# Kernel tuning notes

Measured on AMD Instinct MI355X. Metric: run time of the kernel, lower is better.

## Reference

```python
import jax, jax.numpy as jnp
import numpy as np

N_NODES = 100000
N_EDGES = 1200000
NDIM_IN = 64
EDIMS = 64
NDIM_OUT = 64


def setup_inputs() -> dict:
    key = jax.random.key(0)
    k = jax.random.split(key, 8)
    nfeats = jax.random.normal(k[0], (N_NODES, NDIM_IN), dtype=jnp.float32)
    efeats = jax.random.normal(k[1], (N_EDGES, EDIMS), dtype=jnp.float32)
    src = jax.random.randint(k[2], (N_EDGES,), 0, N_NODES)
    dst = jax.random.randint(k[3], (N_EDGES,), 0, N_NODES)
    # Linear layers: y = x @ W + b, W stored [in, out]
    s_msg = 1.0 / np.sqrt(NDIM_IN + EDIMS)
    s_app = 1.0 / np.sqrt(NDIM_IN + NDIM_OUT)
    W_msg = jax.random.normal(k[4], (NDIM_IN + EDIMS, NDIM_OUT), dtype=jnp.float32) * s_msg
    b_msg = jnp.zeros((NDIM_OUT,), dtype=jnp.float32)
    W_apply = jax.random.normal(k[5], (NDIM_IN + NDIM_OUT, NDIM_OUT), dtype=jnp.float32) * s_app
    b_apply = jnp.zeros((NDIM_OUT,), dtype=jnp.float32)
    return {"nfeats": nfeats, "efeats": efeats, "src": src, "dst": dst,
            "W_msg": W_msg, "b_msg": b_msg, "W_apply": W_apply, "b_apply": b_apply}


def reference(nfeats, efeats, src, dst, W_msg, b_msg, W_apply, b_apply):
    # per-edge message: W_msg(cat[h_src, e_h])  -> [E, ndim_out]
    msg_in = jnp.concatenate([nfeats[src], efeats], axis=1)  # [E, ndim_in+edims]
    m = msg_in @ W_msg + b_msg                                # [E, ndim_out]
    # mean aggregation over destination nodes (DGL fn.mean; 0 for isolated nodes)
    msum = jax.ops.segment_sum(m, dst, num_segments=N_NODES)  # [N, ndim_out]
    deg = jax.ops.segment_sum(jnp.ones((m.shape[0], 1), m.dtype), dst,
                              num_segments=N_NODES)           # [N, 1]
    h_neigh = jnp.where(deg > 0, msum / jnp.maximum(deg, 1.0), 0.0)
    # node update: relu(W_apply(cat[h, h_neigh]))
    h = jax.nn.relu(jnp.concatenate([nfeats, h_neigh], axis=1) @ W_apply + b_apply)
    return h
```

## Files before the change

kernel.cpp:

```cpp
#include <hip/hip_runtime.h>

#define N_NODES 100000
#define N_EDGES 1200000
#define D 64
#define SLOTS 48

typedef float    f32x4 __attribute__((ext_vector_type(4)));
typedef _Float16 f16x4 __attribute__((ext_vector_type(4)));


__global__ __launch_bounds__(256) void init_kernel(
    int4* __restrict__ zp, const float* __restrict__ nfeats,
    const float* __restrict__ W_msg, const float* __restrict__ b_msg,
    const float* __restrict__ W_apply, float* __restrict__ Wf,
    float* __restrict__ c1, _Float16* __restrict__ nf16)
{
    int b = blockIdx.x;
    if (b < 98) {
        int i = b * 256 + threadIdx.x;
        if (i < 25000) zp[i] = make_int4(0, 0, 0, 0);
    } else if (b < 227) {
        if (threadIdx.x < 64) {
            int i = b - 98;
            int j = threadIdx.x;
            float acc = 0.f;
            if (i < 128) {
                for (int k = 0; k < 64; ++k)
                    acc = fmaf(W_msg[i * 64 + k], W_apply[(64 + k) * 64 + j], acc);
                Wf[i * 64 + j] = acc;
            } else {
                for (int k = 0; k < 64; ++k)
                    acc = fmaf(b_msg[k], W_apply[(64 + k) * 64 + j], acc);
                c1[j] = acc;
            }
        }
    } else {
        size_t i = (size_t)(b - 227) * 256 + threadIdx.x;
        if (i < (size_t)N_NODES * 16) {
            f32x4 v = *(const f32x4*)(nfeats + i * 4);
            f16x4 h;
            h[0] = (_Float16)v[0]; h[1] = (_Float16)v[1];
            h[2] = (_Float16)v[2]; h[3] = (_Float16)v[3];
            *(f16x4*)(nf16 + i * 4) = h;
        }
    }
}

__global__ __launch_bounds__(256) void scatter_kernel(
    const int* __restrict__ src, const int* __restrict__ dst,
    int* __restrict__ cursor, int2* __restrict__ idx_s)
{
    int e = blockIdx.x * 256 + threadIdx.x;
    if (e >= N_EDGES) return;
    int d = __builtin_nontemporal_load(dst + e);
    int s = __builtin_nontemporal_load(src + e);
    int pos = atomicAdd(&cursor[d], 1);
    if (pos < SLOTS) idx_s[(size_t)d * SLOTS + pos] = make_int2(e, s);
}

__global__ __launch_bounds__(256) void gather_kernel(
    const _Float16* __restrict__ nf16, const float* __restrict__ efeats,
    const int2* __restrict__ idx_s, const int* __restrict__ cursor,
    float* __restrict__ agg_h, float* __restrict__ agg_e)
{
    int w = (int)((blockIdx.x * blockDim.x + threadIdx.x) >> 6);
    int lane = threadIdx.x & 63;
    if (w >= N_NODES) return;
    int r  = lane >> 4;
    int c4 = (lane & 15) << 2;
    const int2* bucket = idx_s + (size_t)w * SLOTS;
    int dgi = min(__builtin_amdgcn_readfirstlane(cursor[w]), SLOTS);
    f32x4 sh = (f32x4)0.f;
    f32x4 se = (f32x4)0.f;
    int full = dgi & ~7;
    for (int i = 0; i < full; i += 8) {
        int2 pA = bucket[i + r];
        int2 pB = bucket[i + 4 + r];
        f32x4 eA = __builtin_nontemporal_load((const f32x4*)(efeats + (size_t)pA.x * D + c4));
        f32x4 eB = __builtin_nontemporal_load((const f32x4*)(efeats + (size_t)pB.x * D + c4));
        f16x4 hA = *(const f16x4*)(nf16 + (size_t)pA.y * D + c4);
        f16x4 hB = *(const f16x4*)(nf16 + (size_t)pB.y * D + c4);
        se += eA + eB;
        #pragma unroll
        for (int q = 0; q < 4; ++q) sh[q] += (float)hA[q] + (float)hB[q];
    }
    if (full < dgi) {
        int iA = full + r, iB = full + 4 + r;
        float mA = (iA < dgi) ? 1.f : 0.f;
        float mB = (iB < dgi) ? 1.f : 0.f;
        int2 pA = bucket[(iA < dgi) ? iA : 0];
        int2 pB = bucket[(iB < dgi) ? iB : 0];
        f32x4 eA = __builtin_nontemporal_load((const f32x4*)(efeats + (size_t)pA.x * D + c4));
        f32x4 eB = __builtin_nontemporal_load((const f32x4*)(efeats + (size_t)pB.x * D + c4));
        f16x4 hA = *(const f16x4*)(nf16 + (size_t)pA.y * D + c4);
        f16x4 hB = *(const f16x4*)(nf16 + (size_t)pB.y * D + c4);
        #pragma unroll
        for (int q = 0; q < 4; ++q) {
            se[q] = fmaf(mA, eA[q], se[q]); sh[q] = fmaf(mA, (float)hA[q], sh[q]);
            se[q] = fmaf(mB, eB[q], se[q]); sh[q] = fmaf(mB, (float)hB[q], sh[q]);
        }
    }
    #pragma unroll
    for (int m = 16; m <= 32; m <<= 1) {
        #pragma unroll
        for (int q = 0; q < 4; ++q) {
            sh[q] += __shfl_xor(sh[q], m);
            se[q] += __shfl_xor(se[q], m);
        }
    }
    if (r == 0)       *(f32x4*)(agg_h + (size_t)w * D + c4) = sh;
    else if (r == 1)  *(f32x4*)(agg_e + (size_t)w * D + c4) = se;
}

__global__ __launch_bounds__(256) void node_update_kernel(
    const float* __restrict__ nfeats, const float* __restrict__ W_apply,
    const float* __restrict__ b_apply, const float* __restrict__ Wf,
    const float* __restrict__ c1, const float* __restrict__ agg_e,
    const int* __restrict__ deg, float* out )
{
    __shared__ float sX[64 * 17];
    __shared__ float sOut[64 * 65];
    int t = threadIdx.x;
    int l = t & 63;
    int jg = __builtin_amdgcn_readfirstlane(t >> 6);
    int node0 = blockIdx.x * 64;
    int node = min(node0 + l, N_NODES - 1);
    int dgi = deg[node];
    float s = dgi > 0 ? 1.f / (float)dgi : 0.f;
    float gate = dgi > 0 ? 1.f : 0.f;

    float accN[16], accX[16];
    #pragma unroll
    for (int j = 0; j < 16; ++j) { accN[j] = 0.f; accX[j] = 0.f; }

    #define STAGE(srcp, kp)                                                   \
    {                                                                         \
        int row = t >> 2, kq = t & 3;                                         \
        int grow = min(node0 + row, N_NODES - 1);                             \
        f32x4 v = *(const f32x4*)((srcp) + (size_t)grow * D + (kp) + kq * 4); \
        sX[row * 17 + kq * 4 + 0] = v[0];                                     \
        sX[row * 17 + kq * 4 + 1] = v[1];                                     \
        sX[row * 17 + kq * 4 + 2] = v[2];                                     \
        sX[row * 17 + kq * 4 + 3] = v[3];                                     \
    }

    #define ACCUM(acc, Wp, kw0)                                               \
    {                                                                         \
        _Pragma("unroll")                                                     \
        for (int g = 0; g < 4; ++g) {                                         \
            float x0 = sX[l * 17 + g * 4 + 0];                                \
            float x1 = sX[l * 17 + g * 4 + 1];                                \
            float x2 = sX[l * 17 + g * 4 + 2];                                \
            float x3 = sX[l * 17 + g * 4 + 3];                                \
            const float* w0 = (Wp) + (size_t)((kw0) + g * 4 + 0) * 64 + jg * 16; \
            const float* w1 = (Wp) + (size_t)((kw0) + g * 4 + 1) * 64 + jg * 16; \
            const float* w2 = (Wp) + (size_t)((kw0) + g * 4 + 2) * 64 + jg * 16; \
            const float* w3 = (Wp) + (size_t)((kw0) + g * 4 + 3) * 64 + jg * 16; \
            _Pragma("unroll")                                                 \
            for (int jj = 0; jj < 16; ++jj) {                                 \
                acc[jj] = fmaf(x0, w0[jj], acc[jj]);                          \
                acc[jj] = fmaf(x1, w1[jj], acc[jj]);                          \
                acc[jj] = fmaf(x2, w2[jj], acc[jj]);                          \
                acc[jj] = fmaf(x3, w3[jj], acc[jj]);                          \
            }                                                                 \
        }                                                                     \
    }

    for (int p = 0; p < 4; ++p) {
        STAGE(nfeats, p * 16);
        __syncthreads();
        ACCUM(accN, W_apply, p * 16);
        __syncthreads();
    }
    for (int p = 0; p < 8; ++p) {
        const float* srcp = (p < 4) ? out : agg_e;
        STAGE(srcp, (p & 3) * 16);
        __syncthreads();
        ACCUM(accX, Wf, p * 16);
        __syncthreads();
    }

    #pragma unroll
    for (int jj = 0; jj < 16; ++jj) {
        int j = jg * 16 + jj;
        sOut[l * 65 + j] = fmaxf(accN[jj] + s * accX[jj] + gate * c1[j] + b_apply[j], 0.f);
    }
    __syncthreads();

    #pragma unroll
    for (int rr = 0; rr < 16; ++rr) {
        int row = jg * 16 + rr;
        int nd = node0 + row;
        if (nd < N_NODES) out[(size_t)nd * D + l] = sOut[row * 65 + l];
    }
    #undef STAGE
    #undef ACCUM
}

extern "C" void kernel_launch(void* const* d_in, const int* in_sizes, int n_in,
                              void* d_out, int out_size, void* d_ws, size_t ws_size,
                              hipStream_t stream) {
    const float* nfeats  = (const float*)d_in[0];
    const float* efeats  = (const float*)d_in[1];
    const int*   src     = (const int*)d_in[2];
    const int*   dst     = (const int*)d_in[3];
    const float* W_msg   = (const float*)d_in[4];
    const float* b_msg   = (const float*)d_in[5];
    const float* W_apply = (const float*)d_in[6];
    const float* b_apply = (const float*)d_in[7];
    float* out = (float*)d_out;

    int*      cursor = (int*)d_ws;
    float*    Wf     = (float*)(cursor + 100352);
    float*    c1     = Wf + 128 * 64;
    _Float16* nf16   = (_Float16*)(c1 + 64);
    int2*     idx_s  = (int2*)(nf16 + (size_t)N_NODES * D);
    float*    agg_e  = (float*)(idx_s + (size_t)N_NODES * SLOTS);

    init_kernel<<<98 + 129 + 6250, 256, 0, stream>>>(
        (int4*)d_ws, nfeats, W_msg, b_msg, W_apply, Wf, c1, nf16);

    int eb = (N_EDGES + 255) / 256;
    scatter_kernel<<<eb, 256, 0, stream>>>(src, dst, cursor, idx_s);

    gather_kernel<<<N_NODES / 4, 256, 0, stream>>>(
        nf16, efeats, idx_s, cursor, out , agg_e);

    node_update_kernel<<<(N_NODES + 63) / 64, 256, 0, stream>>>(
        nfeats, W_apply, b_apply, Wf, c1, agg_e, cursor, out);
}
```

Before: 217.4 us.

## Fuse node update into gather and precompute the self-feature projection in init

The self term nfeats@W_apply+b_apply is now computed in the init kernel, alongside the fp16 conversion, and written to a Qa buffer. The separate node_update kernel is removed. Each gather wave now multiplies its aggregated sums by the fused Wf matrix held in LDS, using cross-lane shuffles, and writes the final relu output directly. This drops a kernel launch and the round trip of the agg_h/agg_e buffers. In exchange, every 512-thread gather block loads a 32KB weight copy into LDS, which adds per-block staging cost and may lower occupancy.

Measured after the change: 439.5 us. 2.02x slower.

```diff
diff --git a/kernel.cpp b/kernel.cpp
--- a/kernel.cpp
+++ b/kernel.cpp
@@ -12,14 +12,19 @@
 __global__ __launch_bounds__(256) void init_kernel(
     int4* __restrict__ zp, const float* __restrict__ nfeats,
     const float* __restrict__ W_msg, const float* __restrict__ b_msg,
-    const float* __restrict__ W_apply, float* __restrict__ Wf,
-    float* __restrict__ c1, _Float16* __restrict__ nf16)
+    const float* __restrict__ W_apply, const float* __restrict__ b_apply,
+    float* __restrict__ Wf, float* __restrict__ c1,
+    _Float16* __restrict__ nf16, float* __restrict__ Qa)
 {
+    __shared__ float sX[64 * 17];
+    __shared__ float sOut[64 * 65];
     int b = blockIdx.x;
     if (b < 98) {
         int i = b * 256 + threadIdx.x;
         if (i < 25000) zp[i] = make_int4(0, 0, 0, 0);
-    } else if (b < 227) {
+        return;
+    }
+    if (b < 227) {
         if (threadIdx.x < 64) {
             int i = b - 98;
             int j = threadIdx.x;
@@ -34,15 +39,62 @@
                 c1[j] = acc;
             }
         }
-    } else {
-        size_t i = (size_t)(b - 227) * 256 + threadIdx.x;
-        if (i < (size_t)N_NODES * 16) {
-            f32x4 v = *(const f32x4*)(nfeats + i * 4);
+        return;
+    }
+    int node0 = (b - 227) * 64;
+    int t = threadIdx.x;
+    int l = t & 63;
+    int jg = __builtin_amdgcn_readfirstlane(t >> 6);
+    float accN[16];
+    #pragma unroll
+    for (int j = 0; j < 16; ++j) accN[j] = 0.f;
+
+    for (int p = 0; p < 4; ++p) {
+        {
+            int row = t >> 2, kq = t & 3;
+            int grow = min(node0 + row, N_NODES - 1);
+            f32x4 v = *(const f32x4*)(nfeats + (size_t)grow * D + p * 16 + kq * 4);
+            sX[row * 17 + kq * 4 + 0] = v[0];
+            sX[row * 17 + kq * 4 + 1] = v[1];
+            sX[row * 17 + kq * 4 + 2] = v[2];
+            sX[row * 17 + kq * 4 + 3] = v[3];
             f16x4 h;
             h[0] = (_Float16)v[0]; h[1] = (_Float16)v[1];
             h[2] = (_Float16)v[2]; h[3] = (_Float16)v[3];
-            *(f16x4*)(nf16 + i * 4) = h;
-        }
+            *(f16x4*)(nf16 + (size_t)grow * D + p * 16 + kq * 4) = h;
+        }
+        __syncthreads();
+        #pragma unroll
+        for (int g = 0; g < 4; ++g) {
+            float x0 = sX[l * 17 + g * 4 + 0];
+            float x1 = sX[l * 17 + g * 4 + 1];
+            float x2 = sX[l * 17 + g * 4 + 2];
+            float x3 = sX[l * 17 + g * 4 + 3];
+            const float* w0 = W_apply + (size_t)(p * 16 + g * 4 + 0) * 64 + jg * 16;
+            const float* w1 = W_apply + (size_t)(p * 16 + g * 4 + 1) * 64 + jg * 16;
+            const float* w2 = W_apply + (size_t)(p * 16 + g * 4 + 2) * 64 + jg * 16;
+            const float* w3 = W_apply + (size_t)(p * 16 + g * 4 + 3) * 64 + jg * 16;
+            #pragma unroll
+            for (int jj = 0; jj < 16; ++jj) {
+                accN[jj] = fmaf(x0, w0[jj], accN[jj]);
+                accN[jj] = fmaf(x1, w1[jj], accN[jj]);
+                accN[jj] = fmaf(x2, w2[jj], accN[jj]);
+                accN[jj] = fmaf(x3, w3[jj], accN[jj]);
+            }
+        }
+        __syncthreads();
+    }
+    #pragma unroll
+    for (int jj = 0; jj < 16; ++jj) {
+        int j = jg * 16 + jj;
+        sOut[l * 65 + j] = accN[jj] + b_apply[j];
+    }
+    __syncthreads();
+    #pragma unroll
+    for (int rr = 0; rr < 16; ++rr) {
+        int row = jg * 16 + rr;
+        int nd = node0 + row;
+        if (nd < N_NODES) Qa[(size_t)nd * D + l] = sOut[row * 65 + l];
     }
 }
 
@@ -58,13 +110,22 @@
     if (pos < SLOTS) idx_s[(size_t)d * SLOTS + pos] = make_int2(e, s);
 }
 
-__global__ __launch_bounds__(256) void gather_kernel(
+__global__ __launch_bounds__(512) void gather_kernel(
     const _Float16* __restrict__ nf16, const float* __restrict__ efeats,
     const int2* __restrict__ idx_s, const int* __restrict__ cursor,
-    float* __restrict__ agg_h, float* __restrict__ agg_e)
+    const float* __restrict__ Wf, const float* __restrict__ c1,
+    const float* __restrict__ Qa, float* __restrict__ out)
 {
-    int w = (int)((blockIdx.x * blockDim.x + threadIdx.x) >> 6);
-    int lane = threadIdx.x & 63;
+    __shared__ float sWf[128 * 64];
+    __shared__ float sC1[64];
+    int t = threadIdx.x;
+    #pragma unroll
+    for (int i = 0; i < 16; ++i) sWf[i * 512 + t] = Wf[i * 512 + t];
+    if (t < 64) sC1[t] = c1[t];
+    __syncthreads();
+
+    int w = blockIdx.x * 8 + (t >> 6);
+    int lane = t & 63;
     if (w >= N_NODES) return;
     int r  = lane >> 4;
     int c4 = (lane & 15) << 2;
@@ -108,93 +169,22 @@
             se[q] += __shfl_xor(se[q], m);
         }
     }
-    if (r == 0)       *(f32x4*)(agg_h + (size_t)w * D + c4) = sh;
-    else if (r == 1)  *(f32x4*)(agg_e + (size_t)w * D + c4) = se;
-}
-
-__global__ __launch_bounds__(256) void node_update_kernel(
-    const float* __restrict__ nfeats, const float* __restrict__ W_apply,
-    const float* __restrict__ b_apply, const float* __restrict__ Wf,
-    const float* __restrict__ c1, const float* __restrict__ agg_e,
-    const int* __restrict__ deg, float* out )
-{
-    __shared__ float sX[64 * 17];
-    __shared__ float sOut[64 * 65];
-    int t = threadIdx.x;
-    int l = t & 63;
-    int jg = __builtin_amdgcn_readfirstlane(t >> 6);
-    int node0 = blockIdx.x * 64;
-    int node = min(node0 + l, N_NODES - 1);
-    int dgi = deg[node];
-    float s = dgi > 0 ? 1.f / (float)dgi : 0.f;
-    float gate = dgi > 0 ? 1.f : 0.f;
-
-    float accN[16], accX[16];
-    #pragma unroll
-    for (int j = 0; j < 16; ++j) { accN[j] = 0.f; accX[j] = 0.f; }
-
-    #define STAGE(srcp, kp)                                                   \
-    {                                                                         \
-        int row = t >> 2, kq = t & 3;                                         \
-        int grow = min(node0 + row, N_NODES - 1);                             \
-        f32x4 v = *(const f32x4*)((srcp) + (size_t)grow * D + (kp) + kq * 4); \
-        sX[row * 17 + kq * 4 + 0] = v[0];                                     \
-        sX[row * 17 + kq * 4 + 1] = v[1];                                     \
-        sX[row * 17 + kq * 4 + 2] = v[2];                                     \
-        sX[row * 17 + kq * 4 + 3] = v[3];                                     \
-    }
-
-    #define ACCUM(acc, Wp, kw0)                                               \
-    {                                                                         \
-        _Pragma("unroll")                                                     \
-        for (int g = 0; g < 4; ++g) {                                         \
-            float x0 = sX[l * 17 + g * 4 + 0];                                \
-            float x1 = sX[l * 17 + g * 4 + 1];                                \
-            float x2 = sX[l * 17 + g * 4 + 2];                                \
-            float x3 = sX[l * 17 + g * 4 + 3];                                \
-            const float* w0 = (Wp) + (size_t)((kw0) + g * 4 + 0) * 64 + jg * 16; \
-            const float* w1 = (Wp) + (size_t)((kw0) + g * 4 + 1) * 64 + jg * 16; \
-            const float* w2 = (Wp) + (size_t)((kw0) + g * 4 + 2) * 64 + jg * 16; \
-            const float* w3 = (Wp) + (size_t)((kw0) + g * 4 + 3) * 64 + jg * 16; \
-            _Pragma("unroll")                                                 \
-            for (int jj = 0; jj < 16; ++jj) {                                 \
-                acc[jj] = fmaf(x0, w0[jj], acc[jj]);                          \
-                acc[jj] = fmaf(x1, w1[jj], acc[jj]);                          \
-                acc[jj] = fmaf(x2, w2[jj], acc[jj]);                          \
-                acc[jj] = fmaf(x3, w3[jj], acc[jj]);                          \
-            }                                                                 \
-        }                                                                     \
-    }
-
-    for (int p = 0; p < 4; ++p) {
-        STAGE(nfeats, p * 16);
-        __syncthreads();
-        ACCUM(accN, W_apply, p * 16);
-        __syncthreads();
-    }
-    for (int p = 0; p < 8; ++p) {
-        const float* srcp = (p < 4) ? out : agg_e;
-        STAGE(srcp, (p & 3) * 16);
-        __syncthreads();
-        ACCUM(accX, Wf, p * 16);
-        __syncthreads();
-    }
-
-    #pragma unroll
-    for (int jj = 0; jj < 16; ++jj) {
-        int j = jg * 16 + jj;
-        sOut[l * 65 + j] = fmaxf(accN[jj] + s * accX[jj] + gate * c1[j] + b_apply[j], 0.f);
-    }
-    __syncthreads();
-
-    #pragma unroll
-    for (int rr = 0; rr < 16; ++rr) {
-        int row = jg * 16 + rr;
-        int nd = node0 + row;
-        if (nd < N_NODES) out[(size_t)nd * D + l] = sOut[row * 65 + l];
-    }
-    #undef STAGE
-    #undef ACCUM
+
+    float y = 0.f;
+    #pragma unroll
+    for (int c = 0; c < 16; ++c) {
+        #pragma unroll
+        for (int q = 0; q < 4; ++q) {
+            float xs = __shfl(sh[q], c);
+            float xe = __shfl(se[q], c);
+            y = fmaf(xs, sWf[(c * 4 + q) * 64 + lane], y);
+            y = fmaf(xe, sWf[(64 + c * 4 + q) * 64 + lane], y);
+        }
+    }
+
+    float res = Qa[(size_t)w * D + lane];
+    if (dgi > 0) res += y / (float)dgi + sC1[lane];
+    out[(size_t)w * D + lane] = fmaxf(res, 0.f);
 }
 
 extern "C" void kernel_launch(void* const* d_in, const int* in_sizes, int n_in,
@@ -214,18 +204,15 @@
     float*    Wf     = (float*)(cursor + 100352);
     float*    c1     = Wf + 128 * 64;
     _Float16* nf16   = (_Float16*)(c1 + 64);
-    int2*     idx_s  = (int2*)(nf16 + (size_t)N_NODES * D);
-    float*    agg_e  = (float*)(idx_s + (size_t)N_NODES * SLOTS);
-
-    init_kernel<<<98 + 129 + 6250, 256, 0, stream>>>(
-        (int4*)d_ws, nfeats, W_msg, b_msg, W_apply, Wf, c1, nf16);
+    float*    Qa     = (float*)(nf16 + (size_t)N_NODES * D);
+    int2*     idx_s  = (int2*)(Qa + (size_t)N_NODES * D);
+
+    init_kernel<<<98 + 129 + 1563, 256, 0, stream>>>(
+        (int4*)d_ws, nfeats, W_msg, b_msg, W_apply, b_apply, Wf, c1, nf16, Qa);
 
     int eb = (N_EDGES + 255) / 256;
     scatter_kernel<<<eb, 256, 0, stream>>>(src, dst, cursor, idx_s);
 
-    gather_kernel<<<N_NODES / 4, 256, 0, stream>>>(
-        nf16, efeats, idx_s, cursor, out , agg_e);
-
-    node_update_kernel<<<(N_NODES + 63) / 64, 256, 0, stream>>>(
-        nfeats, W_apply, b_apply, Wf, c1, agg_e, cursor, out);
-}
+    gather_kernel<<<(N_NODES + 7) / 8, 512, 0, stream>>>(
+        nf16, efeats, idx_s, cursor, Wf, c1, Qa, out);
+}
```

## Move nfeats@W_apply GEMM into init kernel and prefetch bucket indices in gather

Applied to the files above, without the earlier changes.

The init kernel now converts nfeats to fp16 and also computes the self term nfeats@W_apply+b_apply per 64-node tile, writing it to a new workspace buffer Qa. This shortens node_update, which now only does the aggregated part and adds Qa before the ReLU. The gather loop also software-prefetches the next pair of bucket indices. In exchange, Qa costs an extra 25.6MB write and read round-trip through global memory, and init blocks use more shared memory and registers.

After: 232.1 us. +6.8%, slower.

```diff
diff --git a/kernel.cpp b/kernel.cpp
--- a/kernel.cpp
+++ b/kernel.cpp
@@ -12,14 +12,19 @@
 __global__ __launch_bounds__(256) void init_kernel(
     int4* __restrict__ zp, const float* __restrict__ nfeats,
     const float* __restrict__ W_msg, const float* __restrict__ b_msg,
-    const float* __restrict__ W_apply, float* __restrict__ Wf,
-    float* __restrict__ c1, _Float16* __restrict__ nf16)
-{
+    const float* __restrict__ W_apply, const float* __restrict__ b_apply,
+    float* __restrict__ Wf, float* __restrict__ c1,
+    _Float16* __restrict__ nf16, float* __restrict__ Qa)
+{
+    __shared__ float sX[64 * 17];
+    __shared__ float sOut[64 * 65];
     int b = blockIdx.x;
     if (b < 98) {
         int i = b * 256 + threadIdx.x;
         if (i < 25000) zp[i] = make_int4(0, 0, 0, 0);
-    } else if (b < 227) {
+        return;
+    }
+    if (b < 227) {
         if (threadIdx.x < 64) {
             int i = b - 98;
             int j = threadIdx.x;
@@ -34,15 +39,62 @@
                 c1[j] = acc;
             }
         }
-    } else {
-        size_t i = (size_t)(b - 227) * 256 + threadIdx.x;
-        if (i < (size_t)N_NODES * 16) {
-            f32x4 v = *(const f32x4*)(nfeats + i * 4);
+        return;
+    }
+    int node0 = (b - 227) * 64;
+    int t = threadIdx.x;
+    int l = t & 63;
+    int jg = __builtin_amdgcn_readfirstlane(t >> 6);
+    float accN[16];
+    #pragma unroll
+    for (int j = 0; j < 16; ++j) accN[j] = 0.f;
+
+    for (int p = 0; p < 4; ++p) {
+        {
+            int row = t >> 2, kq = t & 3;
+            int grow = min(node0 + row, N_NODES - 1);
+            f32x4 v = *(const f32x4*)(nfeats + (size_t)grow * D + p * 16 + kq * 4);
+            sX[row * 17 + kq * 4 + 0] = v[0];
+            sX[row * 17 + kq * 4 + 1] = v[1];
+            sX[row * 17 + kq * 4 + 2] = v[2];
+            sX[row * 17 + kq * 4 + 3] = v[3];
             f16x4 h;
             h[0] = (_Float16)v[0]; h[1] = (_Float16)v[1];
             h[2] = (_Float16)v[2]; h[3] = (_Float16)v[3];
-            *(f16x4*)(nf16 + i * 4) = h;
-        }
+            *(f16x4*)(nf16 + (size_t)grow * D + p * 16 + kq * 4) = h;
+        }
+        __syncthreads();
+        #pragma unroll
+        for (int g = 0; g < 4; ++g) {
+            float x0 = sX[l * 17 + g * 4 + 0];
+            float x1 = sX[l * 17 + g * 4 + 1];
+            float x2 = sX[l * 17 + g * 4 + 2];
+            float x3 = sX[l * 17 + g * 4 + 3];
+            const float* w0 = W_apply + (size_t)(p * 16 + g * 4 + 0) * 64 + jg * 16;
+            const float* w1 = W_apply + (size_t)(p * 16 + g * 4 + 1) * 64 + jg * 16;
+            const float* w2 = W_apply + (size_t)(p * 16 + g * 4 + 2) * 64 + jg * 16;
+            const float* w3 = W_apply + (size_t)(p * 16 + g * 4 + 3) * 64 + jg * 16;
+            #pragma unroll
+            for (int jj = 0; jj < 16; ++jj) {
+                accN[jj] = fmaf(x0, w0[jj], accN[jj]);
+                accN[jj] = fmaf(x1, w1[jj], accN[jj]);
+                accN[jj] = fmaf(x2, w2[jj], accN[jj]);
+                accN[jj] = fmaf(x3, w3[jj], accN[jj]);
+            }
+        }
+        __syncthreads();
+    }
+    #pragma unroll
+    for (int jj = 0; jj < 16; ++jj) {
+        int j = jg * 16 + jj;
+        sOut[l * 65 + j] = accN[jj] + b_apply[j];
+    }
+    __syncthreads();
+    #pragma unroll
+    for (int rr = 0; rr < 16; ++rr) {
+        int row = jg * 16 + rr;
+        int nd = node0 + row;
+        if (nd < N_NODES) Qa[(size_t)nd * D + l] = sOut[row * 65 + l];
     }
 }
 
@@ -73,16 +125,21 @@
     f32x4 sh = (f32x4)0.f;
     f32x4 se = (f32x4)0.f;
     int full = dgi & ~7;
-    for (int i = 0; i < full; i += 8) {
-        int2 pA = bucket[i + r];
-        int2 pB = bucket[i + 4 + r];
-        f32x4 eA = __builtin_nontemporal_load((const f32x4*)(efeats + (size_t)pA.x * D + c4));
-        f32x4 eB = __builtin_nontemporal_load((const f32x4*)(efeats + (size_t)pB.x * D + c4));
-        f16x4 hA = *(const f16x4*)(nf16 + (size_t)pA.y * D + c4);
-        f16x4 hB = *(const f16x4*)(nf16 + (size_t)pB.y * D + c4);
-        se += eA + eB;
-        #pragma unroll
-        for (int q = 0; q < 4; ++q) sh[q] += (float)hA[q] + (float)hB[q];
+    if (full > 0) {
+        int2 q0 = bucket[r];
+        int2 q1 = bucket[4 + r];
+        for (int i = 0; i < full; i += 8) {
+            int2 p0 = q0, p1 = q1;
+            int nxt = i + 8;
+            if (nxt < full) { q0 = bucket[nxt + r]; q1 = bucket[nxt + 4 + r]; }
+            f32x4 eA = __builtin_nontemporal_load((const f32x4*)(efeats + (size_t)p0.x * D + c4));
+            f32x4 eB = __builtin_nontemporal_load((const f32x4*)(efeats + (size_t)p1.x * D + c4));
+            f16x4 hA = *(const f16x4*)(nf16 + (size_t)p0.y * D + c4);
+            f16x4 hB = *(const f16x4*)(nf16 + (size_t)p1.y * D + c4);
+            se += eA + eB;
+            #pragma unroll
+            for (int q = 0; q < 4; ++q) sh[q] += (float)hA[q] + (float)hB[q];
+        }
     }
     if (full < dgi) {
         int iA = full + r, iB = full + 4 + r;
@@ -113,8 +170,7 @@
 }
 
 __global__ __launch_bounds__(256) void node_update_kernel(
-    const float* __restrict__ nfeats, const float* __restrict__ W_apply,
-    const float* __restrict__ b_apply, const float* __restrict__ Wf,
+    const float* __restrict__ Qa, const float* __restrict__ Wf,
     const float* __restrict__ c1, const float* __restrict__ agg_e,
     const int* __restrict__ deg, float* out )
 {
@@ -129,9 +185,9 @@
     float s = dgi > 0 ? 1.f / (float)dgi : 0.f;
     float gate = dgi > 0 ? 1.f : 0.f;
 
-    float accN[16], accX[16];
-    #pragma unroll
-    for (int j = 0; j < 16; ++j) { accN[j] = 0.f; accX[j] = 0.f; }
+    float accX[16];
+    #pragma unroll
+    for (int j = 0; j < 16; ++j) accX[j] = 0.f;
 
     #define STAGE(srcp, kp)                                                   \
     {                                                                         \
@@ -166,12 +222,6 @@
         }                                                                     \
     }
 
-    for (int p = 0; p < 4; ++p) {
-        STAGE(nfeats, p * 16);
-        __syncthreads();
-        ACCUM(accN, W_apply, p * 16);
-        __syncthreads();
-    }
     for (int p = 0; p < 8; ++p) {
         const float* srcp = (p < 4) ? out : agg_e;
         STAGE(srcp, (p & 3) * 16);
@@ -183,7 +233,7 @@
     #pragma unroll
     for (int jj = 0; jj < 16; ++jj) {
         int j = jg * 16 + jj;
-        sOut[l * 65 + j] = fmaxf(accN[jj] + s * accX[jj] + gate * c1[j] + b_apply[j], 0.f);
+        sOut[l * 65 + j] = s * accX[jj] + gate * c1[j];
     }
     __syncthreads();
 
@@ -191,7 +241,10 @@
     for (int rr = 0; rr < 16; ++rr) {
         int row = jg * 16 + rr;
         int nd = node0 + row;
-        if (nd < N_NODES) out[(size_t)nd * D + l] = sOut[row * 65 + l];
+        if (nd < N_NODES) {
+            float q = Qa[(size_t)nd * D + l];
+            out[(size_t)nd * D + l] = fmaxf(q + sOut[row * 65 + l], 0.f);
+        }
     }
     #undef STAGE
     #undef ACCUM
@@ -214,11 +267,12 @@
     float*    Wf     = (float*)(cursor + 100352);
     float*    c1     = Wf + 128 * 64;
     _Float16* nf16   = (_Float16*)(c1 + 64);
-    int2*     idx_s  = (int2*)(nf16 + (size_t)N_NODES * D);
+    float*    Qa     = (float*)(nf16 + (size_t)N_NODES * D);
+    int2*     idx_s  = (int2*)(Qa + (size_t)N_NODES * D);
     float*    agg_e  = (float*)(idx_s + (size_t)N_NODES * SLOTS);
 
-    init_kernel<<<98 + 129 + 6250, 256, 0, stream>>>(
-        (int4*)d_ws, nfeats, W_msg, b_msg, W_apply, Wf, c1, nf16);
+    init_kernel<<<98 + 129 + 1563, 256, 0, stream>>>(
+        (int4*)d_ws, nfeats, W_msg, b_msg, W_apply, b_apply, Wf, c1, nf16, Qa);
 
     int eb = (N_EDGES + 255) / 256;
     scatter_kernel<<<eb, 256, 0, stream>>>(src, dst, cursor, idx_s);
@@ -227,5 +281,5 @@
         nf16, efeats, idx_s, cursor, out , agg_e);
 
     node_update_kernel<<<(N_NODES + 63) / 64, 256, 0, stream>>>(
-        nfeats, W_apply, b_apply, Wf, c1, agg_e, cursor, out);
-}
+        Qa, Wf, c1, agg_e, cursor, out);
+}
```
